# Optimization experiments

Measured on AMD Instinct MI355X. Metric: run time of the kernel, lower is better.

## Reference

```python
import jax, jax.numpy as jnp
import numpy as np

N = 100000      # nodes
E = 1600000     # edges (avg degree 16)
G = 1000        # graphs in batch
F_IN = 128      # num_features
C = 10          # num_classes
EPS = 1e-5


def setup_inputs() -> dict:
    key = jax.random.key(0)
    ks = jax.random.split(key, 12)
    w = lambda k, shape: jax.random.normal(k, shape, jnp.float32) * 0.05
    return {
        'x': jax.random.normal(ks[0], (N, F_IN), jnp.float32),
        'edge_index': jax.random.randint(ks[1], (2, E), 0, N, jnp.int32),
        'edge_weights': jax.random.randint(ks[2], (E,), 0, 2, jnp.int32),
        'batch': jnp.sort(jax.random.randint(ks[3], (N,), 0, G, jnp.int32)),
        'num_graphs': G,
        # initial MLP: Linear(128,32)+BN+ReLU, Linear(32,32)+BN+ReLU
        'W1': w(ks[4], (F_IN, 32)), 'b1': jnp.zeros(32), 'g1': jnp.ones(32), 'bt1': jnp.zeros(32),
        'W2': w(ks[5], (32, 32)), 'b2': jnp.zeros(32), 'g2': jnp.ones(32), 'bt2': jnp.zeros(32),
        'Wl0': w(ks[6], (32, C)), 'bl0': jnp.zeros(C),   # initial_linear
        'Wg1': w(ks[7], (32, 64)), 'bg1': jnp.zeros(64),  # GCNConv 1
        'Wl1': w(ks[8], (64, C)), 'bl1': jnp.zeros(C),
        'Wg2': w(ks[9], (64, 64)), 'bg2': jnp.zeros(64),  # GCNConv 2
        'Wl2': w(ks[10], (64, C)), 'bl2': jnp.zeros(C),
    }


def _bn(h, gamma, beta):
    # BatchNorm1d in training mode: biased batch statistics over nodes
    mu = h.mean(0)
    var = ((h - mu) ** 2).mean(0)
    return gamma * (h - mu) * jax.lax.rsqrt(var + EPS) + beta


def _gcn(h_in, row, col, w, W, b):
    # PyG GCNConv with self-loops: D^{-1/2}(A+I)D^{-1/2} X W + b,
    # edges with mask weight 0 contribute nothing (incl. to degree).
    n = h_in.shape[0]
    h = h_in @ W
    deg = jax.ops.segment_sum(w, col, num_segments=n) + 1.0  # +1 self-loop
    dinv = jax.lax.rsqrt(deg)
    norm = w * dinv[row] * dinv[col]                  # [E]
    agg = jax.ops.segment_sum(h[row] * norm[:, None], col, num_segments=n)
    agg = agg + h * (dinv * dinv)[:, None]            # self-loop term
    return agg + b


def _pool_max(h, batch, num_graphs):
    # torch_scatter scatter_max readout; empty segments -> 0
    p = jax.ops.segment_max(h, batch, num_segments=num_graphs)
    return jnp.where(jnp.isfinite(p), p, 0.0)


def reference(x, edge_index, edge_weights, batch, num_graphs,
              W1, b1, g1, bt1, W2, b2, g2, bt2, Wl0, bl0,
              Wg1, bg1, Wl1, bl1, Wg2, bg2, Wl2, bl2):
    row, col = edge_index[0], edge_index[1]
    w = (edge_weights == 1).astype(x.dtype)  # boolean edge mask as 0/1 weight
    # initial MLP (dropout treated as identity for deterministic reference)
    h = jax.nn.relu(_bn(x @ W1 + b1, g1, bt1))
    h = jax.nn.relu(_bn(h @ W2 + b2, g2, bt2))
    out = _pool_max(h @ Wl0 + bl0, batch, num_graphs)
    # layer 1
    h = _gcn(h, row, col, w, Wg1, bg1)
    out = out + _pool_max(h, batch, num_graphs) @ Wl1 + bl1
    # layer 2
    h = _gcn(h, row, col, w, Wg2, bg2)
    out = out + _pool_max(h, batch, num_graphs) @ Wl2 + bl2
    return out
```

## Files before the change

### kernel.cpp

```cpp
#include <hip/hip_runtime.h>

#define NN 100000
#define EE 1600000
#define GG 1000
#define BN_EPS 1e-5f
#define NTB 782
#define SLOT 64

__device__ __forceinline__ unsigned encf(float f){
  unsigned u = __float_as_uint(f);
  return (u & 0x80000000u) ? ~u : (u | 0x80000000u);
}
__device__ __forceinline__ float dec0(unsigned e){
  unsigned u = (e & 0x80000000u) ? (e & 0x7fffffffu) : ~e;
  float f = __uint_as_float(u);
  return isfinite(f) ? f : 0.0f;
}
__device__ __forceinline__ unsigned short f2bf(float f){
  unsigned u = __float_as_uint(f);
  u += 0x7FFFu + ((u >> 16) & 1u);
  return (unsigned short)(u >> 16);
}
__device__ __forceinline__ float bf2f(unsigned short s){
  return __uint_as_float(((unsigned)s) << 16);
}

#define STEP4(AX, WV) \
  acc[0][0]=fmaf(a0.AX,WV.x,acc[0][0]); acc[0][1]=fmaf(a0.AX,WV.y,acc[0][1]); \
  acc[0][2]=fmaf(a0.AX,WV.z,acc[0][2]); acc[0][3]=fmaf(a0.AX,WV.w,acc[0][3]); \
  acc[1][0]=fmaf(a1.AX,WV.x,acc[1][0]); acc[1][1]=fmaf(a1.AX,WV.y,acc[1][1]); \
  acc[1][2]=fmaf(a1.AX,WV.z,acc[1][2]); acc[1][3]=fmaf(a1.AX,WV.w,acc[1][3]); \
  acc[2][0]=fmaf(a2.AX,WV.x,acc[2][0]); acc[2][1]=fmaf(a2.AX,WV.y,acc[2][1]); \
  acc[2][2]=fmaf(a2.AX,WV.z,acc[2][2]); acc[2][3]=fmaf(a2.AX,WV.w,acc[2][3]); \
  acc[3][0]=fmaf(a3.AX,WV.x,acc[3][0]); acc[3][1]=fmaf(a3.AX,WV.y,acc[3][1]); \
  acc[3][2]=fmaf(a3.AX,WV.z,acc[3][2]); acc[3][3]=fmaf(a3.AX,WV.w,acc[3][3]);

__global__ void k_scatter(const int* __restrict__ ei, const int* __restrict__ ew,
                          int* __restrict__ fill, int* __restrict__ csr,
                          const float* __restrict__ x, unsigned short* __restrict__ Xb){
  const int t = blockIdx.x*256 + threadIdx.x;
  if (t < EE && ew[t] == 1){
    int c = ei[EE + t];
    int pos = atomicAdd(&fill[c], 1);
    if (pos < SLOT) csr[(size_t)c*SLOT + pos] = ei[t];
  }
  const size_t base = (size_t)t * 2;
  #pragma unroll
  for (int i = 0; i < 2; i++){
    const size_t idx = base + i;
    if (idx < (size_t)NN*32){
      float4 v = ((const float4*)x)[idx];
      ushort4 u; u.x=f2bf(v.x); u.y=f2bf(v.y); u.z=f2bf(v.z); u.w=f2bf(v.w);
      ((ushort4*)Xb)[idx] = u;
    }
  }
}

__global__ __launch_bounds__(256) void k_gemm1(const unsigned short* __restrict__ Xb,
    const float* __restrict__ W1, const float* __restrict__ b1,
    unsigned short* __restrict__ Y1b, float* __restrict__ stats){
  __shared__ unsigned short xs[128*136];
  __shared__ unsigned short Ws[128*32];
  __shared__ float red[64];
  const int tid = threadIdx.x;
  if (tid < 64) red[tid] = 0.f;
  #pragma unroll
  for (int j = 0; j < 4; j++){
    int idx = tid + j*256;
    int kk = idx >> 3, cc = idx & 7;
    float4 w = ((const float4*)W1)[(size_t)kk*8 + cc];
    ushort4 u; u.x=f2bf(w.x); u.y=f2bf(w.y); u.z=f2bf(w.z); u.w=f2bf(w.w);
    *(ushort4*)&Ws[kk*32 + cc*4] = u;
  }
  const long rowbase = (long)blockIdx.x*128;
  for (int j = tid; j < 4096; j += 256){
    int rr = j >> 5, kk = j & 31;
    long gr = rowbase + rr;
    ushort4 u = (gr < NN) ? ((const ushort4*)Xb)[gr*32 + kk] : ushort4{0,0,0,0};
    *(ushort4*)&xs[rr*136 + kk*4] = u;
  }
  __syncthreads();
  const int rg = tid >> 3, cg = tid & 7;
  const float4 bv = ((const float4*)b1)[cg];
  float acc[4][4];
  #pragma unroll
  for (int i = 0; i < 4; i++){ acc[i][0]=bv.x; acc[i][1]=bv.y; acc[i][2]=bv.z; acc[i][3]=bv.w; }
  #pragma unroll 4
  for (int k = 0; k < 128; k += 4){
    const ushort4 u0 = *(const ushort4*)&xs[(rg     )*136 + k];
    const ushort4 u1 = *(const ushort4*)&xs[(rg + 32)*136 + k];
    const ushort4 u2 = *(const ushort4*)&xs[(rg + 64)*136 + k];
    const ushort4 u3 = *(const ushort4*)&xs[(rg + 96)*136 + k];
    float4 a0, a1, a2, a3;
    a0.x=bf2f(u0.x); a0.y=bf2f(u0.y); a0.z=bf2f(u0.z); a0.w=bf2f(u0.w);
    a1.x=bf2f(u1.x); a1.y=bf2f(u1.y); a1.z=bf2f(u1.z); a1.w=bf2f(u1.w);
    a2.x=bf2f(u2.x); a2.y=bf2f(u2.y); a2.z=bf2f(u2.z); a2.w=bf2f(u2.w);
    a3.x=bf2f(u3.x); a3.y=bf2f(u3.y); a3.z=bf2f(u3.z); a3.w=bf2f(u3.w);
    const ushort4 wu0 = *(const ushort4*)&Ws[(k+0)*32 + cg*4];
    const ushort4 wu1 = *(const ushort4*)&Ws[(k+1)*32 + cg*4];
    const ushort4 wu2 = *(const ushort4*)&Ws[(k+2)*32 + cg*4];
    const ushort4 wu3 = *(const ushort4*)&Ws[(k+3)*32 + cg*4];
    float4 w0, w1, w2, w3;
    w0.x=bf2f(wu0.x); w0.y=bf2f(wu0.y); w0.z=bf2f(wu0.z); w0.w=bf2f(wu0.w);
    w1.x=bf2f(wu1.x); w1.y=bf2f(wu1.y); w1.z=bf2f(wu1.z); w1.w=bf2f(wu1.w);
    w2.x=bf2f(wu2.x); w2.y=bf2f(wu2.y); w2.z=bf2f(wu2.z); w2.w=bf2f(wu2.w);
    w3.x=bf2f(wu3.x); w3.y=bf2f(wu3.y); w3.z=bf2f(wu3.z); w3.w=bf2f(wu3.w);
    STEP4(x, w0) STEP4(y, w1) STEP4(z, w2) STEP4(w, w3)
  }
  float s[4] = {0,0,0,0}, q[4] = {0,0,0,0};
  #pragma unroll
  for (int i = 0; i < 4; i++){
    const long r = rowbase + rg + 32*i;
    if (r < NN){
      ushort4 o; o.x=f2bf(acc[i][0]); o.y=f2bf(acc[i][1]); o.z=f2bf(acc[i][2]); o.w=f2bf(acc[i][3]);
      ((ushort4*)Y1b)[r*8 + cg] = o;
      #pragma unroll
      for (int j = 0; j < 4; j++){ s[j] += acc[i][j]; q[j] += acc[i][j]*acc[i][j]; }
    }
  }
  __syncthreads();
  #pragma unroll
  for (int j = 0; j < 4; j++){
    atomicAdd(&red[cg*4+j], s[j]);
    atomicAdd(&red[32+cg*4+j], q[j]);
  }
  __syncthreads();
  if (tid < 64) atomicAdd(&stats[tid], red[tid]);
}

__global__ __launch_bounds__(256) void k_mlp2(const unsigned short* __restrict__ Y1b,
    const float* __restrict__ W2, const float* __restrict__ b2,
    const float* __restrict__ g1, const float* __restrict__ bt1,
    float* __restrict__ stats, unsigned short* __restrict__ Y2b){
  __shared__ float ht[128*36];
  __shared__ float Ws[32*32];
  __shared__ float red[64];
  __shared__ float scs[32], shs[32];
  const int tid = threadIdx.x;
  ((float4*)Ws)[tid] = ((const float4*)W2)[tid];
  if (tid < 64) red[tid] = 0.f;
  if (tid < 32){
    float mean = stats[tid] * (1.0f/NN);
    float var  = stats[32 + tid] * (1.0f/NN) - mean*mean;
    float sH = g1[tid] * rsqrtf(fmaxf(var, 0.0f) + BN_EPS);
    scs[tid] = sH; shs[tid] = bt1[tid] - mean*sH;
  }
  __syncthreads();
  const long rowbase = (long)blockIdx.x*128;
  for (int j = tid; j < 1024; j += 256){
    int rr = j >> 3, kk = j & 7;
    long gr = rowbase + rr;
    ushort4 u = (gr < NN) ? ((const ushort4*)Y1b)[gr*8 + kk] : ushort4{0,0,0,0};
    float4 v;
    v.x = fmaxf(fmaf(bf2f(u.x), scs[kk*4+0], shs[kk*4+0]), 0.f);
    v.y = fmaxf(fmaf(bf2f(u.y), scs[kk*4+1], shs[kk*4+1]), 0.f);
    v.z = fmaxf(fmaf(bf2f(u.z), scs[kk*4+2], shs[kk*4+2]), 0.f);
    v.w = fmaxf(fmaf(bf2f(u.w), scs[kk*4+3], shs[kk*4+3]), 0.f);
    *(float4*)&ht[rr*36 + kk*4] = v;
  }
  __syncthreads();
  const int rg = tid >> 3, cg = tid & 7;
  const float4 bv = ((const float4*)b2)[cg];
  float acc[4][4];
  #pragma unroll
  for (int i = 0; i < 4; i++){ acc[i][0]=bv.x; acc[i][1]=bv.y; acc[i][2]=bv.z; acc[i][3]=bv.w; }
  #pragma unroll
  for (int k = 0; k < 32; k += 4){
    const float4 a0 = *(const float4*)&ht[(rg     )*36 + k];
    const float4 a1 = *(const float4*)&ht[(rg + 32)*36 + k];
    const float4 a2 = *(const float4*)&ht[(rg + 64)*36 + k];
    const float4 a3 = *(const float4*)&ht[(rg + 96)*36 + k];
    const float4 w0 = *(const float4*)&Ws[(k+0)*32 + cg*4];
    const float4 w1 = *(const float4*)&Ws[(k+1)*32 + cg*4];
    const float4 w2 = *(const float4*)&Ws[(k+2)*32 + cg*4];
    const float4 w3 = *(const float4*)&Ws[(k+3)*32 + cg*4];
    STEP4(x, w0) STEP4(y, w1) STEP4(z, w2) STEP4(w, w3)
  }
  float s[4] = {0,0,0,0}, q[4] = {0,0,0,0};
  #pragma unroll
  for (int i = 0; i < 4; i++){
    const long r = rowbase + rg + 32*i;
    if (r < NN){
      ushort4 o; o.x=f2bf(acc[i][0]); o.y=f2bf(acc[i][1]); o.z=f2bf(acc[i][2]); o.w=f2bf(acc[i][3]);
      ((ushort4*)Y2b)[r*8 + cg] = o;
      #pragma unroll
      for (int j = 0; j < 4; j++){ s[j] += acc[i][j]; q[j] += acc[i][j]*acc[i][j]; }
    }
  }
  __syncthreads();
  #pragma unroll
  for (int j = 0; j < 4; j++){
    atomicAdd(&red[cg*4+j], s[j]);
    atomicAdd(&red[32+cg*4+j], q[j]);
  }
  __syncthreads();
  if (tid < 64) atomicAdd(&stats[128 + tid], red[tid]);
}

__global__ __launch_bounds__(256) void k_layer0(const unsigned short* __restrict__ Y2b,
    const float* __restrict__ stats, const float* __restrict__ g2,
    const float* __restrict__ bt2, const float* __restrict__ Wg1,
    const float* __restrict__ Wl0, const float* __restrict__ bl0,
    const int* __restrict__ fill, const int* __restrict__ batch,
    unsigned short* __restrict__ Hs1, unsigned* __restrict__ Pool0){
  __shared__ float hs[32*36];
  __shared__ float Wg[32*64];
  __shared__ float Wl[320];
  __shared__ float bl[10];
  __shared__ float scs[32], shs[32];
  const int tid = threadIdx.x;
  ((float4*)Wg)[tid]       = ((const float4*)Wg1)[tid];
  ((float4*)Wg)[tid + 256] = ((const float4*)Wg1)[tid + 256];
  for (int j = tid; j < 320; j += 256) Wl[j] = Wl0[j];
  if (tid < 10)  bl[tid] = bl0[tid];
  if (tid < 32){
    float mean = stats[128 + tid] * (1.0f/NN);
    float var  = stats[160 + tid] * (1.0f/NN) - mean*mean;
    float s = g2[tid] * rsqrtf(fmaxf(var, 0.0f) + BN_EPS);
    scs[tid] = s; shs[tid] = bt2[tid] - mean*s;
  }
  __syncthreads();
  {
    const int rr = tid >> 3, kk = tid & 7;
    const float4 sc = *(const float4*)&scs[kk*4];
    const float4 sh = *(const float4*)&shs[kk*4];
    ushort4 u = ((const ushort4*)Y2b)[(size_t)blockIdx.x*256 + tid];
    float4 v;
    v.x = fmaxf(fmaf(bf2f(u.x), sc.x, sh.x), 0.f);
    v.y = fmaxf(fmaf(bf2f(u.y), sc.y, sh.y), 0.f);
    v.z = fmaxf(fmaf(bf2f(u.z), sc.z, sh.z), 0.f);
    v.w = fmaxf(fmaf(bf2f(u.w), sc.w, sh.w), 0.f);
    *(float4*)&hs[rr*36 + kk*4] = v;
  }
  __syncthreads();
  const int w = tid >> 6, f = tid & 63;
  for (int i = 0; i < 8; i++){
    const int r = w*8 + i;
    const int row = blockIdx.x*32 + r;
    const float* hr = &hs[r*36];
    float acc = 0.f;
    #pragma unroll
    for (int k = 0; k < 32; k++) acc += hr[k]*Wg[k*64 + f];
    const float dv = rsqrtf((float)fill[row] + 1.0f);
    Hs1[(size_t)row*64 + f] = f2bf(acc * dv);
    if (f < 10){
      float p = bl[f];
      #pragma unroll
      for (int k = 0; k < 32; k++) p += hr[k]*Wl[k*10 + f];
      atomicMax(&Pool0[batch[row]*10 + f], encf(p));
    }
  }
}

__device__ __forceinline__ void gather2(const unsigned short* __restrict__ Hs,
    const int* __restrict__ csr, int sA, int eA, int sB, int eB, int f,
    float& accA, float& accB){
  int jA = sA, jB = sB;
  while (jA + 3 < eA && jB + 3 < eB){
    const int a0 = csr[jA], a1 = csr[jA+1], a2 = csr[jA+2], a3 = csr[jA+3];
    const int b0 = csr[jB], b1 = csr[jB+1], b2 = csr[jB+2], b3 = csr[jB+3];
    float tA0 = bf2f(Hs[(size_t)a0*64 + f]);
    float tA1 = bf2f(Hs[(size_t)a1*64 + f]);
    float tA2 = bf2f(Hs[(size_t)a2*64 + f]);
    float tA3 = bf2f(Hs[(size_t)a3*64 + f]);
    float tB0 = bf2f(Hs[(size_t)b0*64 + f]);
    float tB1 = bf2f(Hs[(size_t)b1*64 + f]);
    float tB2 = bf2f(Hs[(size_t)b2*64 + f]);
    float tB3 = bf2f(Hs[(size_t)b3*64 + f]);
    accA += (tA0 + tA1) + (tA2 + tA3);
    accB += (tB0 + tB1) + (tB2 + tB3);
    jA += 4; jB += 4;
  }
  for (; jA + 3 < eA; jA += 4){
    const int a0 = csr[jA], a1 = csr[jA+1], a2 = csr[jA+2], a3 = csr[jA+3];
    float t0 = bf2f(Hs[(size_t)a0*64 + f]);
    float t1 = bf2f(Hs[(size_t)a1*64 + f]);
    float t2 = bf2f(Hs[(size_t)a2*64 + f]);
    float t3 = bf2f(Hs[(size_t)a3*64 + f]);
    accA += (t0 + t1) + (t2 + t3);
  }
  for (; jB + 3 < eB; jB += 4){
    const int b0 = csr[jB], b1 = csr[jB+1], b2 = csr[jB+2], b3 = csr[jB+3];
    float t0 = bf2f(Hs[(size_t)b0*64 + f]);
    float t1 = bf2f(Hs[(size_t)b1*64 + f]);
    float t2 = bf2f(Hs[(size_t)b2*64 + f]);
    float t3 = bf2f(Hs[(size_t)b3*64 + f]);
    accB += (t0 + t1) + (t2 + t3);
  }
  for (; jA < eA; jA++) accA += bf2f(Hs[(size_t)csr[jA]*64 + f]);
  for (; jB < eB; jB++) accB += bf2f(Hs[(size_t)csr[jB]*64 + f]);
}

__device__ __forceinline__ void pool_epilogue8(float hA, float hB, int w, int f,
    int cA, int cB, const int* __restrict__ batch, unsigned* __restrict__ Pool,
    float (*sm)[64], int* sb){
  sm[w*2][f] = hA; sm[w*2+1][f] = hB;
  if (f == 0){ sb[w*2] = batch[cA]; sb[w*2+1] = batch[cB]; }
  __syncthreads();
  if (w == 0){
    if (sb[0] == sb[7]){
      float m = fmaxf(fmaxf(fmaxf(sm[0][f], sm[1][f]), fmaxf(sm[2][f], sm[3][f])),
                      fmaxf(fmaxf(sm[4][f], sm[5][f]), fmaxf(sm[6][f], sm[7][f])));
      atomicMax(&Pool[sb[0]*64 + f], encf(m));
    } else {
      #pragma unroll
      for (int i = 0; i < 8; i++)
        atomicMax(&Pool[sb[i]*64 + f], encf(sm[i][f]));
    }
  }
}

__global__ __launch_bounds__(256) void k_agg1(const unsigned short* __restrict__ Hs,
    const int* __restrict__ fill, const int* __restrict__ csr,
    const float* __restrict__ bias, const int* __restrict__ batch,
    unsigned short* __restrict__ H2b, unsigned* __restrict__ Pool){
  __shared__ float sm[8][64];
  __shared__ int sb[8];
  const int w = threadIdx.x >> 6, f = threadIdx.x & 63;
  const int cA = blockIdx.x*8 + w*2, cB = cA + 1;
  const int fA = fill[cA], fB = fill[cB];
  const int sA = cA*SLOT, nA = min(fA, SLOT);
  const int sB = cB*SLOT, nB = min(fB, SLOT);
  float accA = 0.f, accB = 0.f;
  gather2(Hs, csr, sA, sA + nA, sB, sB + nB, f, accA, accB);
  const float dA = rsqrtf((float)fA + 1.0f), dB = rsqrtf((float)fB + 1.0f);
  const float bf = bias[f];
  const float hA = fmaf(accA + bf2f(Hs[(size_t)cA*64 + f]), dA, bf);
  const float hB = fmaf(accB + bf2f(Hs[(size_t)cB*64 + f]), dB, bf);
  H2b[(size_t)cA*64 + f] = f2bf(hA);
  H2b[(size_t)cB*64 + f] = f2bf(hB);
  pool_epilogue8(hA, hB, w, f, cA, cB, batch, Pool, sm, sb);
}

__global__ __launch_bounds__(256) void k_agg2(const unsigned short* __restrict__ Hs,
    const int* __restrict__ fill, const int* __restrict__ csr,
    const float* __restrict__ bias, const int* __restrict__ batch,
    unsigned* __restrict__ Pool){
  __shared__ float sm[8][64];
  __shared__ int sb[8];
  const int w = threadIdx.x >> 6, f = threadIdx.x & 63;
  const int cA = blockIdx.x*8 + w*2, cB = cA + 1;
  const int fA = fill[cA], fB = fill[cB];
  const int sA = cA*SLOT, nA = min(fA, SLOT);
  const int sB = cB*SLOT, nB = min(fB, SLOT);
  float accA = 0.f, accB = 0.f;
  gather2(Hs, csr, sA, sA + nA, sB, sB + nB, f, accA, accB);
  const float dA = rsqrtf((float)fA + 1.0f), dB = rsqrtf((float)fB + 1.0f);
  const float bf = bias[f];
  const float hA = fmaf(accA + bf2f(Hs[(size_t)cA*64 + f]), dA, bf);
  const float hB = fmaf(accB + bf2f(Hs[(size_t)cB*64 + f]), dB, bf);
  pool_epilogue8(hA, hB, w, f, cA, cB, batch, Pool, sm, sb);
}

__global__ __launch_bounds__(256) void k_layer1(const unsigned short* __restrict__ H2b,
    const float* __restrict__ Wg2, const int* __restrict__ fill,
    unsigned short* __restrict__ Hs2){
  __shared__ float as[32*68];
  __shared__ float Wg[64*64];
  const int tid = threadIdx.x;
  #pragma unroll
  for (int j = 0; j < 4; j++) ((float4*)Wg)[tid + j*256] = ((const float4*)Wg2)[tid + j*256];
  {
    const int rr = tid >> 3, kk = tid & 7;
    ushort4 v0 = ((const ushort4*)H2b)[(size_t)blockIdx.x*512 + tid*2];
    ushort4 v1 = ((const ushort4*)H2b)[(size_t)blockIdx.x*512 + tid*2 + 1];
    float* dst = &as[rr*68 + kk*8];
    dst[0]=bf2f(v0.x); dst[1]=bf2f(v0.y); dst[2]=bf2f(v0.z); dst[3]=bf2f(v0.w);
    dst[4]=bf2f(v1.x); dst[5]=bf2f(v1.y); dst[6]=bf2f(v1.z); dst[7]=bf2f(v1.w);
  }
  __syncthreads();
  const int w = tid >> 6, f = tid & 63;
  for (int i = 0; i < 8; i++){
    const int r = w*8 + i;
    const int row = blockIdx.x*32 + r;
    const float* ar = &as[r*68];
    float acc = 0.f;
    #pragma unroll
    for (int k = 0; k < 64; k++) acc += ar[k]*Wg[k*64 + f];
    Hs2[(size_t)row*64 + f] = f2bf(acc * rsqrtf((float)fill[row] + 1.0f));
  }
}

__global__ __launch_bounds__(256) void k_final(const unsigned* __restrict__ P0,
    const unsigned* __restrict__ P1, const unsigned* __restrict__ P2,
    const float* __restrict__ Wl1, const float* __restrict__ bl1,
    const float* __restrict__ Wl2, const float* __restrict__ bl2,
    float* __restrict__ out){
  const int t = blockIdx.x*256 + threadIdx.x;
  const int g = t >> 4, c = t & 15;
  if (g >= GG || c >= 10) return;
  float acc = dec0(P0[g*10 + c]) + bl1[c] + bl2[c];
  for (int f = 0; f < 64; f++){
    acc += dec0(P1[g*64 + f]) * Wl1[f*10 + c];
    acc += dec0(P2[g*64 + f]) * Wl2[f*10 + c];
  }
  out[g*10 + c] = acc;
}

extern "C" void kernel_launch(void* const* d_in, const int* in_sizes, int n_in,
                              void* d_out, int out_size, void* d_ws, size_t ws_size,
                              hipStream_t stream){
  const float* x   = (const float*)d_in[0];
  const int*   ei  = (const int*)d_in[1];
  const int*   ew  = (const int*)d_in[2];
  const int*   bat = (const int*)d_in[3];
  const float* W1  = (const float*)d_in[5],  *b1  = (const float*)d_in[6];
  const float* g1  = (const float*)d_in[7],  *bt1 = (const float*)d_in[8];
  const float* W2  = (const float*)d_in[9],  *b2  = (const float*)d_in[10];
  const float* g2  = (const float*)d_in[11], *bt2 = (const float*)d_in[12];
  const float* Wl0 = (const float*)d_in[13], *bl0 = (const float*)d_in[14];
  const float* Wg1 = (const float*)d_in[15], *bg1 = (const float*)d_in[16];
  const float* Wl1 = (const float*)d_in[17], *bl1 = (const float*)d_in[18];
  const float* Wg2 = (const float*)d_in[19], *bg2 = (const float*)d_in[20];
  const float* Wl2 = (const float*)d_in[21], *bl2 = (const float*)d_in[22];

  float* ws = (float*)d_ws;
  const size_t oFill  = 0;
  const size_t oStats = NN;
  const size_t oP0    = oStats + 256;
  const size_t oP1    = oP0 + (size_t)GG*10;
  const size_t oP2    = oP1 + (size_t)GG*64;
  const size_t oZEnd  = oP2 + (size_t)GG*64;
  const size_t oCsr   = oZEnd;
  const size_t oR1    = oCsr + (size_t)NN*SLOT;
  const size_t oR2    = oR1 + (size_t)NN*16;
  const size_t oR3    = oR2 + (size_t)NN*16;
  const size_t oR4    = oR3 + (size_t)NN*32;

  int*   fill  = (int*)(ws + oFill);
  float* stats = ws + oStats;
  unsigned* P0 = (unsigned*)(ws + oP0);
  unsigned* P1 = (unsigned*)(ws + oP1);
  unsigned* P2 = (unsigned*)(ws + oP2);
  int*   csr   = (int*)(ws + oCsr);
  unsigned short* Y1b = (unsigned short*)(ws + oR1);
  unsigned short* Y2b = (unsigned short*)(ws + oR2);
  unsigned short* Xb  = (unsigned short*)(ws + oR3);
  unsigned short* Hs1 = (unsigned short*)(ws + oR3);
  unsigned short* Hs2 = (unsigned short*)(ws + oR3);
  unsigned short* H2b = (unsigned short*)(ws + oR4);

  (void)hipMemsetAsync(d_ws, 0, oZEnd*sizeof(float), stream);

  k_scatter<<<EE/256, 256, 0, stream>>>(ei, ew, fill, csr, x, Xb);
  k_gemm1<<<NTB, 256, 0, stream>>>(Xb, W1, b1, Y1b, stats);
  k_mlp2 <<<NTB, 256, 0, stream>>>(Y1b, W2, b2, g1, bt1, stats, Y2b);
  k_layer0<<<3125, 256, 0, stream>>>(Y2b, stats, g2, bt2, Wg1, Wl0, bl0, fill, bat, Hs1, P0);
  k_agg1 <<<NN/8, 256, 0, stream>>>(Hs1, fill, csr, bg1, bat, H2b, P1);
  k_layer1<<<3125, 256, 0, stream>>>(H2b, Wg2, fill, Hs2);
  k_agg2 <<<NN/8, 256, 0, stream>>>(Hs2, fill, csr, bg2, bat, P2);
  k_final<<<(GG*16 + 255)/256, 256, 0, stream>>>(P0, P1, P2, Wl1, bl1, Wl2, bl2, (float*)d_out);
}
```

Measured before the change: 279.1 us.

## Fuse edge scatter and x-to-bf16 conversion into first GEMM kernel

Merges the CSR edge-scatter kernel and the first MLP GEMM into one launch. Each block scatters 2048 edges, then reads fp32 x directly and converts it to bf16 in shared memory in two K-halves, keeping W1 in fp32. This drops the intermediate bf16 copy of x (a write and a re-read of it) and one launch. In exchange there is an extra sync per K-half and less parallelism for the atomic-heavy scatter phase.

```diff
diff --git a/kernel.cpp b/kernel.cpp
--- a/kernel.cpp
+++ b/kernel.cpp
@@ -35,77 +35,68 @@
   acc[3][0]=fmaf(a3.AX,WV.x,acc[3][0]); acc[3][1]=fmaf(a3.AX,WV.y,acc[3][1]); \
   acc[3][2]=fmaf(a3.AX,WV.z,acc[3][2]); acc[3][3]=fmaf(a3.AX,WV.w,acc[3][3]);
 
-__global__ void k_scatter(const int* __restrict__ ei, const int* __restrict__ ew,
-                          int* __restrict__ fill, int* __restrict__ csr,
-                          const float* __restrict__ x, unsigned short* __restrict__ Xb){
-  const int t = blockIdx.x*256 + threadIdx.x;
-  if (t < EE && ew[t] == 1){
-    int c = ei[EE + t];
-    int pos = atomicAdd(&fill[c], 1);
-    if (pos < SLOT) csr[(size_t)c*SLOT + pos] = ei[t];
-  }
-  const size_t base = (size_t)t * 2;
-  #pragma unroll
-  for (int i = 0; i < 2; i++){
-    const size_t idx = base + i;
-    if (idx < (size_t)NN*32){
-      float4 v = ((const float4*)x)[idx];
-      ushort4 u; u.x=f2bf(v.x); u.y=f2bf(v.y); u.z=f2bf(v.z); u.w=f2bf(v.w);
-      ((ushort4*)Xb)[idx] = u;
-    }
-  }
-}
-
-__global__ __launch_bounds__(256) void k_gemm1(const unsigned short* __restrict__ Xb,
-    const float* __restrict__ W1, const float* __restrict__ b1,
-    unsigned short* __restrict__ Y1b, float* __restrict__ stats){
-  __shared__ unsigned short xs[128*136];
-  __shared__ unsigned short Ws[128*32];
+__global__ __launch_bounds__(256) void k_sg(
+    const int* __restrict__ ei, const int* __restrict__ ew,
+    int* __restrict__ fill, int* __restrict__ csr,
+    const float* __restrict__ x, const float* __restrict__ W1,
+    const float* __restrict__ b1, unsigned short* __restrict__ Y1b,
+    float* __restrict__ stats){
+  __shared__ unsigned short xs[128*72];
+  __shared__ float Ws[64*32];
   __shared__ float red[64];
   const int tid = threadIdx.x;
+  {
+    const size_t ebase = (size_t)blockIdx.x*2048 + tid;
+    #pragma unroll
+    for (int i = 0; i < 8; i++){
+      const size_t e = ebase + (size_t)i*256;
+      if (e < EE && ew[e] == 1){
+        int c = ei[EE + e];
+        int pos = atomicAdd(&fill[c], 1);
+        if (pos < SLOT) csr[(size_t)c*SLOT + pos] = ei[e];
+      }
+    }
+  }
   if (tid < 64) red[tid] = 0.f;
-  #pragma unroll
-  for (int j = 0; j < 4; j++){
-    int idx = tid + j*256;
-    int kk = idx >> 3, cc = idx & 7;
-    float4 w = ((const float4*)W1)[(size_t)kk*8 + cc];
-    ushort4 u; u.x=f2bf(w.x); u.y=f2bf(w.y); u.z=f2bf(w.z); u.w=f2bf(w.w);
-    *(ushort4*)&Ws[kk*32 + cc*4] = u;
-  }
-  const long rowbase = (long)blockIdx.x*128;
-  for (int j = tid; j < 4096; j += 256){
-    int rr = j >> 5, kk = j & 31;
-    long gr = rowbase + rr;
-    ushort4 u = (gr < NN) ? ((const ushort4*)Xb)[gr*32 + kk] : ushort4{0,0,0,0};
-    *(ushort4*)&xs[rr*136 + kk*4] = u;
-  }
-  __syncthreads();
   const int rg = tid >> 3, cg = tid & 7;
   const float4 bv = ((const float4*)b1)[cg];
   float acc[4][4];
   #pragma unroll
   for (int i = 0; i < 4; i++){ acc[i][0]=bv.x; acc[i][1]=bv.y; acc[i][2]=bv.z; acc[i][3]=bv.w; }
-  #pragma unroll 4
-  for (int k = 0; k < 128; k += 4){
-    const ushort4 u0 = *(const ushort4*)&xs[(rg     )*136 + k];
-    const ushort4 u1 = *(const ushort4*)&xs[(rg + 32)*136 + k];
-    const ushort4 u2 = *(const ushort4*)&xs[(rg + 64)*136 + k];
-    const ushort4 u3 = *(const ushort4*)&xs[(rg + 96)*136 + k];
-    float4 a0, a1, a2, a3;
-    a0.x=bf2f(u0.x); a0.y=bf2f(u0.y); a0.z=bf2f(u0.z); a0.w=bf2f(u0.w);
-    a1.x=bf2f(u1.x); a1.y=bf2f(u1.y); a1.z=bf2f(u1.z); a1.w=bf2f(u1.w);
-    a2.x=bf2f(u2.x); a2.y=bf2f(u2.y); a2.z=bf2f(u2.z); a2.w=bf2f(u2.w);
-    a3.x=bf2f(u3.x); a3.y=bf2f(u3.y); a3.z=bf2f(u3.z); a3.w=bf2f(u3.w);
-    const ushort4 wu0 = *(const ushort4*)&Ws[(k+0)*32 + cg*4];
-    const ushort4 wu1 = *(const ushort4*)&Ws[(k+1)*32 + cg*4];
-    const ushort4 wu2 = *(const ushort4*)&Ws[(k+2)*32 + cg*4];
-    const ushort4 wu3 = *(const ushort4*)&Ws[(k+3)*32 + cg*4];
-    float4 w0, w1, w2, w3;
-    w0.x=bf2f(wu0.x); w0.y=bf2f(wu0.y); w0.z=bf2f(wu0.z); w0.w=bf2f(wu0.w);
-    w1.x=bf2f(wu1.x); w1.y=bf2f(wu1.y); w1.z=bf2f(wu1.z); w1.w=bf2f(wu1.w);
-    w2.x=bf2f(wu2.x); w2.y=bf2f(wu2.y); w2.z=bf2f(wu2.z); w2.w=bf2f(wu2.w);
-    w3.x=bf2f(wu3.x); w3.y=bf2f(wu3.y); w3.z=bf2f(wu3.z); w3.w=bf2f(wu3.w);
-    STEP4(x, w0) STEP4(y, w1) STEP4(z, w2) STEP4(w, w3)
+  const long rowbase = (long)blockIdx.x*128;
+  #pragma unroll
+  for (int half = 0; half < 2; half++){
+    __syncthreads();
+    for (int j = tid; j < 512; j += 256){
+      int kk = j >> 3, cc = j & 7;
+      ((float4*)Ws)[j] = ((const float4*)W1)[(size_t)(half*64 + kk)*8 + cc];
+    }
+    for (int j = tid; j < 2048; j += 256){
+      int rr = j >> 4, kk = j & 15;
+      long gr = rowbase + rr;
+      float4 v = (gr < NN) ? ((const float4*)(x + gr*128 + half*64))[kk]
+                           : float4{0.f,0.f,0.f,0.f};
+      ushort4 u; u.x=f2bf(v.x); u.y=f2bf(v.y); u.z=f2bf(v.z); u.w=f2bf(v.w);
+      *(ushort4*)&xs[rr*72 + kk*4] = u;
+    }
+    __syncthreads();
+    #pragma unroll 4
+    for (int k = 0; k < 64; k += 4){
+      const ushort4 u0 = *(const ushort4*)&xs[(rg     )*72 + k];
+      const ushort4 u1 = *(const ushort4*)&xs[(rg + 32)*72 + k];
+      const ushort4 u2 = *(const ushort4*)&xs[(rg + 64)*72 + k];
+      const ushort4 u3 = *(const ushort4*)&xs[(rg + 96)*72 + k];
+      float4 a0, a1, a2, a3;
+      a0.x=bf2f(u0.x); a0.y=bf2f(u0.y); a0.z=bf2f(u0.z); a0.w=bf2f(u0.w);
+      a1.x=bf2f(u1.x); a1.y=bf2f(u1.y); a1.z=bf2f(u1.z); a1.w=bf2f(u1.w);
+      a2.x=bf2f(u2.x); a2.y=bf2f(u2.y); a2.z=bf2f(u2.z); a2.w=bf2f(u2.w);
+      a3.x=bf2f(u3.x); a3.y=bf2f(u3.y); a3.z=bf2f(u3.z); a3.w=bf2f(u3.w);
+      const float4 w0 = *(const float4*)&Ws[(k+0)*32 + cg*4];
+      const float4 w1 = *(const float4*)&Ws[(k+1)*32 + cg*4];
+      const float4 w2 = *(const float4*)&Ws[(k+2)*32 + cg*4];
+      const float4 w3 = *(const float4*)&Ws[(k+3)*32 + cg*4];
+      STEP4(x, w0) STEP4(y, w1) STEP4(z, w2) STEP4(w, w3)
+    }
   }
   float s[4] = {0,0,0,0}, q[4] = {0,0,0,0};
   #pragma unroll
@@ -435,15 +426,13 @@
   int*   csr   = (int*)(ws + oCsr);
   unsigned short* Y1b = (unsigned short*)(ws + oR1);
   unsigned short* Y2b = (unsigned short*)(ws + oR2);
-  unsigned short* Xb  = (unsigned short*)(ws + oR3);
   unsigned short* Hs1 = (unsigned short*)(ws + oR3);
   unsigned short* Hs2 = (unsigned short*)(ws + oR3);
   unsigned short* H2b = (unsigned short*)(ws + oR4);
 
   (void)hipMemsetAsync(d_ws, 0, oZEnd*sizeof(float), stream);
 
-  k_scatter<<<EE/256, 256, 0, stream>>>(ei, ew, fill, csr, x, Xb);
-  k_gemm1<<<NTB, 256, 0, stream>>>(Xb, W1, b1, Y1b, stats);
+  k_sg   <<<NTB, 256, 0, stream>>>(ei, ew, fill, csr, x, W1, b1, Y1b, stats);
   k_mlp2 <<<NTB, 256, 0, stream>>>(Y1b, W2, b2, g1, bt1, stats, Y2b);
   k_layer0<<<3125, 256, 0, stream>>>(Y2b, stats, g2, bt2, Wg1, Wl0, bl0, fill, bat, Hs1, P0);
   k_agg1 <<<NN/8, 256, 0, stream>>>(Hs1, fill, csr, bg1, bat, H2b, P1);
```

New measurement: 278.4 us. About the same (-0.2%).
